# Kernel optimization log

Hardware: AMD Instinct MI355X
Metric: run time of the kernel (lower is better)

The kernel has to match this reference:

```python
import jax, jax.numpy as jnp
import numpy as np

B, C, H, W = 16, 256, 96, 96
SCALES = [0.25, 0.5, 0.75]


def setup_inputs() -> dict:
    key = jax.random.key(0)
    k0, k1, k2, k3, k4, k5 = jax.random.split(key, 6)
    skip = jax.random.normal(k0, (B, C, H, W), dtype=jnp.float32)
    dec = jax.random.normal(k1, (B, C, H, W), dtype=jnp.float32)
    # FEA per-channel edge weight: randn + 0.5 (as in nn.Parameter init)
    w_fea = jax.random.normal(k2, (1, C, 1, 1), dtype=jnp.float32) + 0.5
    # DoG raw sigmas: randn - 0.4 and randn - 0.0
    sigma1 = jax.random.normal(k3, (1, C, 1, 1), dtype=jnp.float32) - 0.4
    sigma2 = jax.random.normal(k4, (1, C, 1, 1), dtype=jnp.float32)
    # 1x1 mixer conv weight, OIHW, no bias
    mixer_w = jax.random.normal(k5, (C, C, 1, 1), dtype=jnp.float32) * 0.05
    return {"skip": skip, "dec": dec, "w_fea": w_fea,
            "sigma1": sigma1, "sigma2": sigma2, "mixer_w": mixer_w}


def _resize(x, h, w):
    # torch F.interpolate(mode='bilinear', align_corners=False) == half-pixel, no antialias
    return jax.image.resize(x, (x.shape[0], x.shape[1], h, w), method="bilinear", antialias=False)


def _fea(y, w_fea):
    h, w = y.shape[2], y.shape[3]
    # multi-scale edge maps: |y - up(down(y))|
    edges = [jnp.abs(y - _resize(_resize(y, int(h * s), int(w * s)), h, w)) for s in SCALES]
    n = len(edges)
    pairs = [(i, j) for i in range(n) for j in range(i + 1, n)]
    m = float(len(pairs))
    w_edge = sum(jnp.abs(edges[i] - edges[j]) for i, j in pairs) / m
    return y + w_fea * w_edge


def _gauss3(sigma_raw):
    # sigma = 2*sigmoid(raw); 3x3 gaussian per channel, normalized
    sig = 2.0 * jax.nn.sigmoid(sigma_raw.reshape(-1))           # (C,)
    coords = jnp.array([-1.0, 0.0, 1.0], dtype=jnp.float32)
    gx, gy = jnp.meshgrid(coords, coords, indexing="ij")
    r2 = gx ** 2 + gy ** 2                                       # (3,3)
    kern = jnp.exp(-r2[None, :, :] / (2.0 * sig[:, None, None] ** 2))
    kern = kern / kern.sum(axis=(1, 2), keepdims=True)
    return kern[:, None, :, :]                                   # (C,1,3,3) OIHW depthwise


def _dwconv3(x, kern):
    return jax.lax.conv_general_dilated(
        x, kern, window_strides=(1, 1), padding="SAME",
        dimension_numbers=("NCHW", "OIHW", "NCHW"),
        feature_group_count=x.shape[1])


def reference(skip, dec, w_fea, sigma1, sigma2, mixer_w):
    y = dec + skip                                   # mode == 'add'
    x_fea = _fea(y, w_fea) + y                       # FEA branch + residual
    dog = _dwconv3(y, _gauss3(sigma1)) - _dwconv3(y, _gauss3(sigma2))
    x_dog = dog + y                                  # DoG branch + residual
    z = x_fea + x_dog
    z = jax.lax.conv_general_dilated(
        z, mixer_w, window_strides=(1, 1), padding="VALID",
        dimension_numbers=("NCHW", "OIHW", "NCHW"))  # 1x1 mixer, no bias
    return z + skip
```

## Files before the change

### kernel.cpp

```cpp
#include <hip/hip_runtime.h>
#include <cstdint>
#include <cmath>

typedef _Float16 half4v __attribute__((ext_vector_type(4)));
typedef _Float16 half8v __attribute__((ext_vector_type(8)));
typedef unsigned short ushort8v __attribute__((ext_vector_type(8)));
typedef float float4v __attribute__((ext_vector_type(4)));

#define NB 16
#define NC 256
#define HW 9216

__global__ __launch_bounds__(512) void stage1_kernel(
    const float* __restrict__ skip, const float* __restrict__ dec,
    const float* __restrict__ wfea, const float* __restrict__ sig1,
    const float* __restrict__ sig2, _Float16* __restrict__ zt) {
    __shared__ __align__(16) float sy[HW];
    __shared__ float d72b[72 * 72];
    __shared__ float d48b[48 * 48];
    __shared__ float d24b[24 * 24];
    __shared__ int   tIA[3][96];
    __shared__ int   tIB[3][96];
    __shared__ float tFR[3][96];

    const int tid = threadIdx.x;
    const int b = blockIdx.x >> 6;
    const int cg = blockIdx.x & 63;

    for (int i = tid; i < 288; i += 512) {
        int s = i / 96, v = i - s * 96;
        float sf = (s == 0) ? 0.25f : (s == 1 ? 0.5f : 0.75f);
        float of = (s == 0) ? 0.375f : (s == 1 ? 0.25f : 0.125f);
        int S = (s == 0) ? 24 : (s == 1 ? 48 : 72);
        float src = (float)v * sf - of;
        float f0 = floorf(src);
        int i0 = (int)f0;
        tFR[s][v] = src - f0;
        tIA[s][v] = i0 < 0 ? 0 : i0;
        tIB[s][v] = (i0 + 1 > S - 1) ? S - 1 : i0 + 1;
    }

    for (int cc = 0; cc < 4; ++cc) {
        const int c = cg * 4 + cc;
        const size_t base = ((size_t)b * NC + c) * HW;
        __syncthreads();
        const float4* dp = (const float4*)(dec + base);
        const float4* sp = (const float4*)(skip + base);
        for (int i = tid; i < HW / 4; i += 512) {
            float4 a = dp[i], s = sp[i];
            float4 v = make_float4(a.x + s.x, a.y + s.y, a.z + s.z, a.w + s.w);
            *(float4*)&sy[i * 4] = v;
        }
        __syncthreads();
        for (int i = tid; i < 48 * 48; i += 512) {
            int oy = i / 48, ox = i - oy * 48;
            const float* r = &sy[oy * 192 + ox * 2];
            d48b[i] = 0.25f * (r[0] + r[1] + r[96] + r[97]);
        }
        for (int i = tid; i < 24 * 24; i += 512) {
            int oy = i / 24, ox = i - oy * 24;
            const float* r = &sy[(4 * oy + 1) * 96 + 4 * ox + 1];
            d24b[i] = 0.25f * (r[0] + r[1] + r[96] + r[97]);
        }
        for (int i = tid; i < 72 * 72; i += 512) {
            int oy = i / 72, ox = i - oy * 72;
            int qy = oy / 3, ry = oy - qy * 3;
            int qx = ox / 3, rx = ox - qx * 3;
            int iy = 4 * qy + ry, ix = 4 * qx + rx;
            float fy = (ry == 0) ? 0.16666667f : (ry == 1 ? 0.5f : 0.83333333f);
            float fx = (rx == 0) ? 0.16666667f : (rx == 1 ? 0.5f : 0.83333333f);
            const float* r0 = &sy[iy * 96 + ix];
            float v0 = r0[0] + fx * (r0[1] - r0[0]);
            float v1 = r0[96] + fx * (r0[97] - r0[96]);
            d72b[i] = v0 + fy * (v1 - v0);
        }
        float wf = wfea[c];
        float sgA = 2.f / (1.f + expf(-sig1[c]));
        float sgB = 2.f / (1.f + expf(-sig2[c]));
        float eA = expf(-0.5f / (sgA * sgA));
        float eB = expf(-0.5f / (sgB * sgB));
        float nA = 1.f + 4.f * eA + 4.f * eA * eA;
        float nB = 1.f + 4.f * eB + 4.f * eB * eB;
        float k0 = 1.f / nA - 1.f / nB;
        float k1 = eA / nA - eB / nB;
        float k2 = eA * eA / nA - eB * eB / nB;
        __syncthreads();
        auto bil = [&](const float* d, int S, int si, int hh, int xx) -> float {
            int ya = tIA[si][hh] * S, yb = tIB[si][hh] * S;
            float fy = tFR[si][hh];
            int xa = tIA[si][xx], xb = tIB[si][xx];
            float fx = tFR[si][xx];
            float a = d[ya + xa], bb = d[ya + xb];
            float cv = d[yb + xa], e = d[yb + xb];
            float t = a + fx * (bb - a);
            float u = cv + fx * (e - cv);
            return t + fy * (u - t);
        };
        for (int p = tid; p < HW; p += 512) {
            int h = p / 96, x = p - h * 96;
            float yv = sy[p];
            float u24 = bil(d24b, 24, 0, h, x);
            float u48 = bil(d48b, 48, 1, h, x);
            float u72 = bil(d72b, 72, 2, h, x);
            float e0 = fabsf(yv - u24);
            float e1 = fabsf(yv - u48);
            float e2 = fabsf(yv - u72);
            float we = (fabsf(e0 - e1) + fabsf(e0 - e2) + fabsf(e1 - e2)) * (1.f / 3.f);
            float up = (h > 0) ? sy[p - 96] : 0.f;
            float dn = (h < 95) ? sy[p + 96] : 0.f;
            float lf = (x > 0) ? sy[p - 1] : 0.f;
            float rt = (x < 95) ? sy[p + 1] : 0.f;
            float ul = (h > 0 && x > 0) ? sy[p - 97] : 0.f;
            float ur = (h > 0 && x < 95) ? sy[p - 95] : 0.f;
            float dl = (h < 95 && x > 0) ? sy[p + 95] : 0.f;
            float dr = (h < 95 && x < 95) ? sy[p + 97] : 0.f;
            float dog = k0 * yv + k1 * (up + dn + lf + rt) + k2 * (ul + ur + dl + dr);
            float z = 3.f * yv + wf * we + dog;
            zt[base + p] = (_Float16)z;
        }
    }
}

__global__ __launch_bounds__(256, 4) void gemm_kernel(
    const _Float16* __restrict__ zt, const float* __restrict__ W,
    const float* __restrict__ skip, float* __restrict__ out) {
    __shared__ __align__(16) _Float16 As[128 * 72];
    __shared__ __align__(16) _Float16 Bs[64 * 72];

    const int tid = threadIdx.x;
    const int bid = blockIdx.x;
    const int ni = bid % 144;
    const int mi = (bid / 144) & 1;
    const int b  = bid / 288;
    const int n0 = ni * 64;
    const int m0 = mi * 128;
    const int lane = tid & 63;
    const int w = tid >> 6;
    const int wm = (w & 1) * 64;
    const int wn = (w >> 1) * 32;
    const int l15 = lane & 15;
    const int quad = lane >> 4;

    float4v acc[4][2];
    #pragma unroll
    for (int i = 0; i < 4; ++i)
        #pragma unroll
        for (int j = 0; j < 2; ++j)
            acc[i][j] = (float4v){0.f, 0.f, 0.f, 0.f};

    for (int kt = 0; kt < 4; ++kt) {
        const int kb = kt * 64;
        __syncthreads();
        #pragma unroll
        for (int p = 0; p < 8; ++p) {
            int idx = tid + p * 256;
            int row = idx >> 4, c4 = (idx & 15) << 2;
            float4 wv = *(const float4*)&W[(m0 + row) * 256 + kb + c4];
            half4v h = { (_Float16)wv.x, (_Float16)wv.y, (_Float16)wv.z, (_Float16)wv.w };
            *(half4v*)&As[row * 72 + c4] = h;
        }
        {
            int ci2 = tid >> 3, nb8 = tid & 7;
            int c0 = 2 * ci2;
            const size_t zrow = ((size_t)b * NC + kb + c0) * HW + n0 + nb8 * 8;
            half8v g0 = *(const half8v*)&zt[zrow];
            half8v g1 = *(const half8v*)&zt[zrow + HW];
            ushort8v u0 = (ushort8v)g0;
            ushort8v u1 = (ushort8v)g1;
            #pragma unroll
            for (int t = 0; t < 8; ++t) {
                int n = nb8 * 8 + t;
                unsigned v = (unsigned)u0[t] | ((unsigned)u1[t] << 16);
                int boff = (n * 144 + c0 * 2) ^ (nb8 << 4);
                *(unsigned*)((char*)Bs + boff) = v;
            }
        }
        __syncthreads();
        #pragma unroll
        for (int q = 0; q < 2; ++q) {
            const int kq = q * 32 + quad * 8;
            half8v af[4], bf[2];
            #pragma unroll
            for (int i = 0; i < 4; ++i)
                af[i] = *(const half8v*)&As[(wm + i * 16 + l15) * 72 + kq];
            #pragma unroll
            for (int j = 0; j < 2; ++j) {
                int n = wn + j * 16 + l15;
                int roff = (n * 144 + kq * 2) ^ (((n >> 3) & 7) << 4);
                bf[j] = *(const half8v*)((const char*)Bs + roff);
            }
            #pragma unroll
            for (int i = 0; i < 4; ++i)
                #pragma unroll
                for (int j = 0; j < 2; ++j)
                    acc[i][j] = __builtin_amdgcn_mfma_f32_16x16x32_f16(af[i], bf[j], acc[i][j], 0, 0, 0);
        }
    }
    #pragma unroll
    for (int i = 0; i < 4; ++i) {
        #pragma unroll
        for (int r = 0; r < 4; ++r) {
            int o = m0 + wm + i * 16 + quad * 4 + r;
            size_t rowbase = ((size_t)b * NC + o) * HW + n0;
            #pragma unroll
            for (int j = 0; j < 2; ++j) {
                int n = wn + j * 16 + l15;
                out[rowbase + n] = acc[i][j][r] + skip[rowbase + n];
            }
        }
    }
}

extern "C" void kernel_launch(void* const* d_in, const int* in_sizes, int n_in,
                              void* d_out, int out_size, void* d_ws, size_t ws_size,
                              hipStream_t stream) {
    const float* skip = (const float*)d_in[0];
    const float* dec  = (const float*)d_in[1];
    const float* wfea = (const float*)d_in[2];
    const float* sg1  = (const float*)d_in[3];
    const float* sg2  = (const float*)d_in[4];
    const float* W    = (const float*)d_in[5];
    float* out = (float*)d_out;
    _Float16* zt = (_Float16*)d_ws;

    stage1_kernel<<<NB * 64, 512, 0, stream>>>(skip, dec, wfea, sg1, sg2, zt);
    gemm_kernel<<<16 * 288, 256, 0, stream>>>(zt, W, skip, out);
}
```

Before: 516.5 us.

## Vectorize stage1 per 4-pixel groups, prefetch next channel, widen GEMM tile to full M

```diff
diff --git a/kernel.cpp b/kernel.cpp
--- a/kernel.cpp
+++ b/kernel.cpp
@@ -6,61 +6,68 @@
 typedef _Float16 half8v __attribute__((ext_vector_type(8)));
 typedef unsigned short ushort8v __attribute__((ext_vector_type(8)));
 typedef float float4v __attribute__((ext_vector_type(4)));
+typedef float float2v __attribute__((ext_vector_type(2)));
 
 #define NB 16
 #define NC 256
 #define HW 9216
 
-__global__ __launch_bounds__(512) void stage1_kernel(
+__global__ __launch_bounds__(512, 4) void stage1_kernel(
     const float* __restrict__ skip, const float* __restrict__ dec,
     const float* __restrict__ wfea, const float* __restrict__ sig1,
     const float* __restrict__ sig2, _Float16* __restrict__ zt) {
     __shared__ __align__(16) float sy[HW];
-    __shared__ float d72b[72 * 72];
-    __shared__ float d48b[48 * 48];
-    __shared__ float d24b[24 * 24];
-    __shared__ int   tIA[3][96];
-    __shared__ int   tIB[3][96];
-    __shared__ float tFR[3][96];
+    __shared__ __align__(16) float d72b[72 * 72];
+    __shared__ __align__(16) float d48b[48 * 48];
+    __shared__ __align__(16) float d24b[24 * 24];
 
     const int tid = threadIdx.x;
     const int b = blockIdx.x >> 6;
     const int cg = blockIdx.x & 63;
 
-    for (int i = tid; i < 288; i += 512) {
-        int s = i / 96, v = i - s * 96;
-        float sf = (s == 0) ? 0.25f : (s == 1 ? 0.5f : 0.75f);
-        float of = (s == 0) ? 0.375f : (s == 1 ? 0.25f : 0.125f);
-        int S = (s == 0) ? 24 : (s == 1 ? 48 : 72);
-        float src = (float)v * sf - of;
-        float f0 = floorf(src);
-        int i0 = (int)f0;
-        tFR[s][v] = src - f0;
-        tIA[s][v] = i0 < 0 ? 0 : i0;
-        tIB[s][v] = (i0 + 1 > S - 1) ? S - 1 : i0 + 1;
+    const float4* dp0 = (const float4*)(dec + ((size_t)b * NC + cg * 4) * HW);
+    const float4* sp0 = (const float4*)(skip + ((size_t)b * NC + cg * 4) * HW);
+    float4 pd[5], ps[5];
+    #pragma unroll
+    for (int it = 0; it < 5; ++it) {
+        int g = tid + it * 512;
+        if (g < 2304) { pd[it] = dp0[g]; ps[it] = sp0[g]; }
     }
 
     for (int cc = 0; cc < 4; ++cc) {
         const int c = cg * 4 + cc;
         const size_t base = ((size_t)b * NC + c) * HW;
         __syncthreads();
-        const float4* dp = (const float4*)(dec + base);
-        const float4* sp = (const float4*)(skip + base);
-        for (int i = tid; i < HW / 4; i += 512) {
-            float4 a = dp[i], s = sp[i];
-            float4 v = make_float4(a.x + s.x, a.y + s.y, a.z + s.z, a.w + s.w);
-            *(float4*)&sy[i * 4] = v;
+        #pragma unroll
+        for (int it = 0; it < 5; ++it) {
+            int g = tid + it * 512;
+            if (g < 2304) {
+                float4 a = pd[it], s = ps[it];
+                float4v v = {a.x + s.x, a.y + s.y, a.z + s.z, a.w + s.w};
+                *(float4v*)&sy[g * 4] = v;
+            }
+        }
+        if (cc < 3) {
+            const float4* dpn = (const float4*)(dec + base + HW);
+            const float4* spn = (const float4*)(skip + base + HW);
+            #pragma unroll
+            for (int it = 0; it < 5; ++it) {
+                int g = tid + it * 512;
+                if (g < 2304) { pd[it] = dpn[g]; ps[it] = spn[g]; }
+            }
         }
         __syncthreads();
         for (int i = tid; i < 48 * 48; i += 512) {
             int oy = i / 48, ox = i - oy * 48;
-            const float* r = &sy[oy * 192 + ox * 2];
-            d48b[i] = 0.25f * (r[0] + r[1] + r[96] + r[97]);
+            float2v a = *(const float2v*)&sy[oy * 192 + ox * 2];
+            float2v bb = *(const float2v*)&sy[oy * 192 + 96 + ox * 2];
+            d48b[i] = 0.25f * (a[0] + a[1] + bb[0] + bb[1]);
         }
         for (int i = tid; i < 24 * 24; i += 512) {
             int oy = i / 24, ox = i - oy * 24;
-            const float* r = &sy[(4 * oy + 1) * 96 + 4 * ox + 1];
-            d24b[i] = 0.25f * (r[0] + r[1] + r[96] + r[97]);
+            float4v t = *(const float4v*)&sy[(4 * oy + 1) * 96 + 4 * ox];
+            float4v u = *(const float4v*)&sy[(4 * oy + 2) * 96 + 4 * ox];
+            d24b[i] = 0.25f * (t[1] + t[2] + u[1] + u[2]);
         }
         for (int i = tid; i < 72 * 72; i += 512) {
             int oy = i / 72, ox = i - oy * 72;
@@ -85,114 +92,173 @@
         float k1 = eA / nA - eB / nB;
         float k2 = eA * eA / nA - eB * eB / nB;
         __syncthreads();
-        auto bil = [&](const float* d, int S, int si, int hh, int xx) -> float {
-            int ya = tIA[si][hh] * S, yb = tIB[si][hh] * S;
-            float fy = tFR[si][hh];
-            int xa = tIA[si][xx], xb = tIB[si][xx];
-            float fx = tFR[si][xx];
-            float a = d[ya + xa], bb = d[ya + xb];
-            float cv = d[yb + xa], e = d[yb + xb];
-            float t = a + fx * (bb - a);
-            float u = cv + fx * (e - cv);
-            return t + fy * (u - t);
-        };
-        for (int p = tid; p < HW; p += 512) {
-            int h = p / 96, x = p - h * 96;
-            float yv = sy[p];
-            float u24 = bil(d24b, 24, 0, h, x);
-            float u48 = bil(d48b, 48, 1, h, x);
-            float u72 = bil(d72b, 72, 2, h, x);
-            float e0 = fabsf(yv - u24);
-            float e1 = fabsf(yv - u48);
-            float e2 = fabsf(yv - u72);
-            float we = (fabsf(e0 - e1) + fabsf(e0 - e2) + fabsf(e1 - e2)) * (1.f / 3.f);
-            float up = (h > 0) ? sy[p - 96] : 0.f;
-            float dn = (h < 95) ? sy[p + 96] : 0.f;
-            float lf = (x > 0) ? sy[p - 1] : 0.f;
-            float rt = (x < 95) ? sy[p + 1] : 0.f;
-            float ul = (h > 0 && x > 0) ? sy[p - 97] : 0.f;
-            float ur = (h > 0 && x < 95) ? sy[p - 95] : 0.f;
-            float dl = (h < 95 && x > 0) ? sy[p + 95] : 0.f;
-            float dr = (h < 95 && x < 95) ? sy[p + 97] : 0.f;
-            float dog = k0 * yv + k1 * (up + dn + lf + rt) + k2 * (ul + ur + dl + dr);
-            float z = 3.f * yv + wf * we + dog;
-            zt[base + p] = (_Float16)z;
+        #pragma unroll 1
+        for (int it = 0; it < 5; ++it) {
+            int g = tid + it * 512;
+            if (g >= 2304) break;
+            int h = g / 24, xg = g - h * 24;
+            int x0 = xg * 4;
+            int rbase = h * 96 + x0;
+            float4v vc = *(const float4v*)&sy[rbase];
+            float lc = (xg > 0) ? sy[rbase - 1] : 0.f;
+            float rc = (xg < 23) ? sy[rbase + 4] : 0.f;
+            float4v vm, vp; float lm, rm, lp, rp;
+            if (h > 0) {
+                vm = *(const float4v*)&sy[rbase - 96];
+                lm = (xg > 0) ? sy[rbase - 97] : 0.f;
+                rm = (xg < 23) ? sy[rbase - 92] : 0.f;
+            } else { vm = (float4v){0.f, 0.f, 0.f, 0.f}; lm = 0.f; rm = 0.f; }
+            if (h < 95) {
+                vp = *(const float4v*)&sy[rbase + 96];
+                lp = (xg > 0) ? sy[rbase + 95] : 0.f;
+                rp = (xg < 23) ? sy[rbase + 100] : 0.f;
+            } else { vp = (float4v){0.f, 0.f, 0.f, 0.f}; lp = 0.f; rp = 0.f; }
+            int i24 = (h - 2) >> 2; int ya24 = i24 < 0 ? 0 : i24; int yb24 = (i24 + 1 > 23) ? 23 : i24 + 1;
+            float fy24 = (h & 2) ? ((h & 1) ? 0.375f : 0.125f) : ((h & 1) ? 0.875f : 0.625f);
+            int i48 = (h - 1) >> 1; int ya48 = i48 < 0 ? 0 : i48; int yb48 = (i48 + 1 > 47) ? 47 : i48 + 1;
+            float fy48 = (h & 1) ? 0.25f : 0.75f;
+            int i72 = (3 * h - 1) >> 2; int ya72 = i72 < 0 ? 0 : i72; int yb72 = (i72 + 1 > 71) ? 71 : i72 + 1;
+            float fy72 = (h & 2) ? ((h & 1) ? 0.125f : 0.375f) : ((h & 1) ? 0.625f : 0.875f);
+            int a24 = xg > 0 ? xg - 1 : 0;
+            int c24c = xg < 23 ? xg + 1 : 23;
+            const float* t24r = &d24b[ya24 * 24];
+            const float* b24r = &d24b[yb24 * 24];
+            float q00 = t24r[a24], q01 = t24r[xg], q02 = t24r[c24c];
+            float q10 = b24r[a24], q11 = b24r[xg], q12 = b24r[c24c];
+            int c48 = 2 * xg;
+            int a48 = c48 > 0 ? c48 - 1 : 0;
+            int e48 = (c48 + 2 > 47) ? 47 : c48 + 2;
+            const float* t48r = &d48b[ya48 * 48];
+            const float* b48r = &d48b[yb48 * 48];
+            float r00 = t48r[a48], r01 = t48r[c48], r02 = t48r[c48 + 1], r03 = t48r[e48];
+            float r10 = b48r[a48], r11 = b48r[c48], r12 = b48r[c48 + 1], r13 = b48r[e48];
+            int c72 = 3 * xg;
+            int a72 = c72 > 0 ? c72 - 1 : 0;
+            int e72 = (c72 + 3 > 71) ? 71 : c72 + 3;
+            const float* t72r = &d72b[ya72 * 72];
+            const float* b72r = &d72b[yb72 * 72];
+            float s00 = t72r[a72], s01 = t72r[c72], s02 = t72r[c72 + 1], s03 = t72r[c72 + 2], s04 = t72r[e72];
+            float s10 = b72r[a72], s11 = b72r[c72], s12 = b72r[c72 + 1], s13 = b72r[c72 + 2], s14 = b72r[e72];
+
+            auto bl2 = [](float ta, float tb, float ba, float bb_, float fx, float fy) {
+                float t = ta + fx * (tb - ta);
+                float u = ba + fx * (bb_ - ba);
+                return t + fy * (u - t);
+            };
+            float u24_0 = bl2(q00, q01, q10, q11, 0.625f, fy24);
+            float u24_1 = bl2(q00, q01, q10, q11, 0.875f, fy24);
+            float u24_2 = bl2(q01, q02, q11, q12, 0.125f, fy24);
+            float u24_3 = bl2(q01, q02, q11, q12, 0.375f, fy24);
+            float u48_0 = bl2(r00, r01, r10, r11, 0.75f, fy48);
+            float u48_1 = bl2(r01, r02, r11, r12, 0.25f, fy48);
+            float u48_2 = bl2(r01, r02, r11, r12, 0.75f, fy48);
+            float u48_3 = bl2(r02, r03, r12, r13, 0.25f, fy48);
+            float u72_0 = bl2(s00, s01, s10, s11, 0.875f, fy72);
+            float u72_1 = bl2(s01, s02, s11, s12, 0.625f, fy72);
+            float u72_2 = bl2(s02, s03, s12, s13, 0.375f, fy72);
+            float u72_3 = bl2(s03, s04, s13, s14, 0.125f, fy72);
+
+            auto pix = [&](float yv, float u24, float u48, float u72,
+                           float ns, float cs) -> _Float16 {
+                float e0 = fabsf(yv - u24);
+                float e1 = fabsf(yv - u48);
+                float e2 = fabsf(yv - u72);
+                float we = (fabsf(e0 - e1) + fabsf(e0 - e2) + fabsf(e1 - e2)) * (1.f / 3.f);
+                float z = 3.f * yv + wf * we + k0 * yv + k1 * ns + k2 * cs;
+                return (_Float16)z;
+            };
+            half4v zv;
+            zv[0] = pix(vc[0], u24_0, u48_0, u72_0, vm[0] + vp[0] + lc + vc[1],
+                        lm + vm[1] + lp + vp[1]);
+            zv[1] = pix(vc[1], u24_1, u48_1, u72_1, vm[1] + vp[1] + vc[0] + vc[2],
+                        vm[0] + vm[2] + vp[0] + vp[2]);
+            zv[2] = pix(vc[2], u24_2, u48_2, u72_2, vm[2] + vp[2] + vc[1] + vc[3],
+                        vm[1] + vm[3] + vp[1] + vp[3]);
+            zv[3] = pix(vc[3], u24_3, u48_3, u72_3, vm[3] + vp[3] + vc[2] + rc,
+                        vm[2] + rm + vp[2] + rp);
+            *(half4v*)&zt[base + (size_t)g * 4] = zv;
         }
     }
 }
 
-__global__ __launch_bounds__(256, 4) void gemm_kernel(
+__global__ __launch_bounds__(256, 3) void gemm_kernel(
     const _Float16* __restrict__ zt, const float* __restrict__ W,
     const float* __restrict__ skip, float* __restrict__ out) {
-    __shared__ __align__(16) _Float16 As[128 * 72];
-    __shared__ __align__(16) _Float16 Bs[64 * 72];
+    __shared__ __align__(16) _Float16 As[256 * 64];
+    __shared__ __align__(16) _Float16 Bs[64 * 64];
 
     const int tid = threadIdx.x;
     const int bid = blockIdx.x;
     const int ni = bid % 144;
-    const int mi = (bid / 144) & 1;
-    const int b  = bid / 288;
+    const int b  = bid / 144;
     const int n0 = ni * 64;
-    const int m0 = mi * 128;
     const int lane = tid & 63;
     const int w = tid >> 6;
-    const int wm = (w & 1) * 64;
-    const int wn = (w >> 1) * 32;
+    const int wm = w * 64;
     const int l15 = lane & 15;
     const int quad = lane >> 4;
 
-    float4v acc[4][2];
+    float4v acc[4][4];
     #pragma unroll
     for (int i = 0; i < 4; ++i)
         #pragma unroll
-        for (int j = 0; j < 2; ++j)
+        for (int j = 0; j < 4; ++j)
             acc[i][j] = (float4v){0.f, 0.f, 0.f, 0.f};
+
+    const int ci2 = tid >> 3, nb8 = tid & 7;
+    const int c0 = 2 * ci2;
+    const size_t zbase = ((size_t)b * NC + c0) * HW + n0 + nb8 * 8;
+    half8v bg0 = *(const half8v*)&zt[zbase];
+    half8v bg1 = *(const half8v*)&zt[zbase + HW];
 
     for (int kt = 0; kt < 4; ++kt) {
         const int kb = kt * 64;
         __syncthreads();
-        #pragma unroll
-        for (int p = 0; p < 8; ++p) {
-            int idx = tid + p * 256;
-            int row = idx >> 4, c4 = (idx & 15) << 2;
-            float4 wv = *(const float4*)&W[(m0 + row) * 256 + kb + c4];
-            half4v h = { (_Float16)wv.x, (_Float16)wv.y, (_Float16)wv.z, (_Float16)wv.w };
-            *(half4v*)&As[row * 72 + c4] = h;
-        }
         {
-            int ci2 = tid >> 3, nb8 = tid & 7;
-            int c0 = 2 * ci2;
-            const size_t zrow = ((size_t)b * NC + kb + c0) * HW + n0 + nb8 * 8;
-            half8v g0 = *(const half8v*)&zt[zrow];
-            half8v g1 = *(const half8v*)&zt[zrow + HW];
-            ushort8v u0 = (ushort8v)g0;
-            ushort8v u1 = (ushort8v)g1;
+            ushort8v u0 = (ushort8v)bg0, u1 = (ushort8v)bg1;
             #pragma unroll
             for (int t = 0; t < 8; ++t) {
                 int n = nb8 * 8 + t;
                 unsigned v = (unsigned)u0[t] | ((unsigned)u1[t] << 16);
-                int boff = (n * 144 + c0 * 2) ^ (nb8 << 4);
+                int boff = (n * 128 + c0 * 2) ^ ((n & 7) << 4);
                 *(unsigned*)((char*)Bs + boff) = v;
             }
         }
-        __syncthreads();
+        #pragma unroll
+        for (int p = 0; p < 16; ++p) {
+            int idx = tid + p * 256;
+            int row = idx >> 4, c4 = (idx & 15) << 2;
+            float4 wv = *(const float4*)&W[row * 256 + kb + c4];
+            half4v hv = { (_Float16)wv.x, (_Float16)wv.y, (_Float16)wv.z, (_Float16)wv.w };
+            int aoff = (row * 128 + c4 * 2) ^ ((row & 7) << 4);
+            *(half4v*)((char*)As + aoff) = hv;
+        }
+        __syncthreads();
+        if (kt < 3) {
+            const size_t znext = zbase + (size_t)(kb + 64) * HW;
+            bg0 = *(const half8v*)&zt[znext];
+            bg1 = *(const half8v*)&zt[znext + HW];
+        }
         #pragma unroll
         for (int q = 0; q < 2; ++q) {
             const int kq = q * 32 + quad * 8;
-            half8v af[4], bf[2];
-            #pragma unroll
-            for (int i = 0; i < 4; ++i)
-                af[i] = *(const half8v*)&As[(wm + i * 16 + l15) * 72 + kq];
-            #pragma unroll
-            for (int j = 0; j < 2; ++j) {
-                int n = wn + j * 16 + l15;
-                int roff = (n * 144 + kq * 2) ^ (((n >> 3) & 7) << 4);
-                bf[j] = *(const half8v*)((const char*)Bs + roff);
+            half8v af[4], bf[4];
+            #pragma unroll
+            for (int i = 0; i < 4; ++i) {
+                int row = wm + i * 16 + l15;
+                int off = (row * 128 + kq * 2) ^ ((row & 7) << 4);
+                af[i] = *(const half8v*)((const char*)As + off);
+            }
+            #pragma unroll
+            for (int j = 0; j < 4; ++j) {
+                int n = j * 16 + l15;
+                int off = (n * 128 + kq * 2) ^ ((n & 7) << 4);
+                bf[j] = *(const half8v*)((const char*)Bs + off);
             }
             #pragma unroll
             for (int i = 0; i < 4; ++i)
                 #pragma unroll
-                for (int j = 0; j < 2; ++j)
+                for (int j = 0; j < 4; ++j)
                     acc[i][j] = __builtin_amdgcn_mfma_f32_16x16x32_f16(af[i], bf[j], acc[i][j], 0, 0, 0);
         }
     }
@@ -200,11 +266,11 @@
     for (int i = 0; i < 4; ++i) {
         #pragma unroll
         for (int r = 0; r < 4; ++r) {
-            int o = m0 + wm + i * 16 + quad * 4 + r;
+            int o = wm + i * 16 + quad * 4 + r;
             size_t rowbase = ((size_t)b * NC + o) * HW + n0;
             #pragma unroll
-            for (int j = 0; j < 2; ++j) {
-                int n = wn + j * 16 + l15;
+            for (int j = 0; j < 4; ++j) {
+                int n = j * 16 + l15;
                 out[rowbase + n] = acc[i][j][r] + skip[rowbase + n];
             }
         }
@@ -224,5 +290,5 @@
     _Float16* zt = (_Float16*)d_ws;
 
     stage1_kernel<<<NB * 64, 512, 0, stream>>>(skip, dec, wfea, sg1, sg2, zt);
-    gemm_kernel<<<16 * 288, 256, 0, stream>>>(zt, W, skip, out);
+    gemm_kernel<<<144 * NB, 256, 0, stream>>>(zt, W, skip, out);
 }
```

Result: faster. 485.6 us (-6.0%).
